# Performance work log

Measured on AMD Instinct MI355X. Metric: run time of the kernel, lower is better.

The kernel has to match this reference:

```python
import jax, jax.numpy as jnp
import numpy as np

B_CAPS, C_CAPS, KSZ, STRIDE, N_ITER = 32, 32, 3, 2, 3


def setup_inputs() -> dict:
    key = jax.random.key(0)
    k1, k2, k3, k4, k5 = jax.random.split(key, 5)
    b, Bc, Cc, Win = 8, B_CAPS, C_CAPS, 13
    pose = 0.5 * jax.random.normal(k1, (b, 16 * Bc, Win, Win), jnp.float32)
    act = 0.05 + 0.9 * jax.random.uniform(k2, (b, Bc, Win, Win), jnp.float32)
    x = jnp.concatenate([pose, act], axis=1)
    W = 0.3 * jax.random.normal(k3, (KSZ, KSZ, Bc, Cc, 4, 4), jnp.float32)
    beta_v = jax.random.normal(k4, (1,), jnp.float32)
    beta_a = jax.random.normal(k5, (1,), jnp.float32)
    lambda_ = jnp.ones((1,), jnp.float32)
    return {"x": x, "W": W, "beta_v": beta_v, "beta_a": beta_a, "lambda_": lambda_}


def _conv_caps(x, W, beta_v, beta_a, lambda_):
    B, C, K, s, n_iter = B_CAPS, C_CAPS, KSZ, STRIDE, N_ITER
    b, Win = x.shape[0], x.shape[2]
    Wout = (Win - K) // s + 1
    # channel layout of pose is (4,4,B) row-major, per the original .view(-1,4,4,B,...)
    pose = x[:, :-B].reshape(b, 4, 4, B, Win, Win)
    act = x[:, -B:]
    ks = jnp.arange(K)
    Iidx = s * jnp.arange(Wout)[None, :] + ks[:, None]  # (K,Wout): i_in = s*x + ki
    Ir = Iidx[:, None, :, None]  # (K,1,Wout,1)
    Ic = Iidx[None, :, None, :]  # (1,K,1,Wout)
    # pose patches: (b,4,4,B,K,K,Wout,Wout); matrix dims are (q=rows, r=cols)
    pp = pose[:, :, :, :, Ir, Ic]
    # votes[n,o,ki,kj,x,y,c,p,r] = sum_q W[ki,kj,o,c,p,q] * pose[n,q,r,o,ki,kj,x,y]
    votes = jnp.einsum('ijocpq,nqroijxy->noijxycpr', W, pp)
    votes = votes.reshape(b, B, K, K, Wout, Wout, C, 16)
    a_patch = act[:, :, Ir, Ic]  # (b,B,K,K,Wout,Wout)
    # original E-step indexes votes at pos = stride*x - i, which is <=0 and wraps
    # (torch negative indexing) to (-ki) % K.  Faithfully reproduce that permutation.
    kperm = (-ks) % K
    votesE = votes[:, :, kperm][:, :, :, kperm]
    # routing weights kept in patch form R[i_in=s*x+ki, j_in=s*y+kj, x, y] -> (ki,kj,x,y);
    # this is exactly the set of R entries the original ever reads or writes.
    Rp = jnp.full((b, B, K, K, Wout, Wout, C), 1.0 / (Wout * Wout * C), x.dtype)
    TWO_PI = np.float32(2.0 * np.pi)
    lam = jnp.reshape(lambda_, ())
    mu = act_out = None
    for it in range(n_iter):
        # ---- M-step ----
        r_hat = Rp * a_patch[..., None]                      # (b,B,K,K,Wo,Wo,C)
        sum_r = r_hat.sum(axis=(1, 2, 3))                    # (b,Wo,Wo,C)
        mu = jnp.einsum('noijxyc,noijxycd->nxycd', r_hat, votes) / sum_r[..., None]
        mu_b = mu[:, None, None, None]                       # (b,1,1,1,Wo,Wo,C,16)
        sigma = jnp.einsum('noijxyc,noijxycd->nxycd', r_hat, (votes - mu_b) ** 2) / sum_r[..., None]
        cost = (beta_v + jnp.log(sigma)) * sum_r[..., None]  # (b,Wo,Wo,C,16)
        act_out = jax.nn.sigmoid(lam * (beta_a - cost.sum(-1)))  # (b,Wo,Wo,C)
        # ---- E-step (skipped on last iter: its R is never read afterwards) ----
        if it < n_iter - 1:
            # original: p = exp(-(V-mu)^2)/sqrt(2*pi*sigma), prod over 16 pose dims
            p = jnp.prod(jnp.exp(-(votesE - mu_b) ** 2) / jnp.sqrt(TWO_PI * sigma[:, None, None, None]), axis=-1)
            p_hat = act_out[:, None, None, None] * p         # (b,B,K,K,Wo,Wo,C)
            T = p_hat.sum(-1)                                # (b,B,K,K,Wo,Wo)
            # normalizer is per (batch, input-type, input-position): scatter-add over
            # all (ki,x),(kj,y) mapping to the same input pixel, summed over C
            D = jnp.zeros((b, B, Win, Win), x.dtype).at[:, :, Ir, Ic].add(T)
            Rp = p_hat / D[:, :, Ir, Ic][..., None]
    mus = mu.transpose(0, 3, 4, 1, 2).reshape(b, C * 16, Wout, Wout)
    acts = act_out.transpose(0, 3, 1, 2)                     # (b,C,Wo,Wo)
    return jnp.concatenate([mus, acts], axis=1)              # (b, C*17, Wo, Wo)


def reference(x, W, beta_v, beta_a, lambda_):
    return _conv_caps(x, W, beta_v, beta_a, lambda_)
```

## Files before the change

kernel.cpp:

```cpp
#include <hip/hip_runtime.h>


typedef float v2f __attribute__((ext_vector_type(2)));
typedef float v4f __attribute__((ext_vector_type(4)));

#define OFF_PHAT 0
#define OFF_D0   2654208
#define OFF_D1   2697472
#define OFF_POST 2740736
#define OFF_ACTT 3432960
#define OFF_WT2  3476224

template <int CTRL>
__device__ __forceinline__ float dppadd(float v) {
  int p = __builtin_amdgcn_update_dpp(0, __float_as_int(v), CTRL, 0xF, 0xF, true);
  return v + __int_as_float(p);
}

__device__ __forceinline__ float wsum64(float v) {
  v = dppadd<0xB1>(v);
  v = dppadd<0x4E>(v);
  v = dppadd<0x141>(v);
  v = dppadd<0x140>(v);
  v = dppadd<0x142>(v);
  v = dppadd<0x143>(v);
  return __int_as_float(__builtin_amdgcn_readlane(__float_as_int(v), 63));
}

__device__ __forceinline__ v2f lo2(v4f a) { return __builtin_shufflevector(a, a, 0, 1); }
__device__ __forceinline__ v2f hi2(v4f a) { return __builtin_shufflevector(a, a, 2, 3); }

__global__ __launch_bounds__(256) void prep_kernel(
    const float* __restrict__ x, const float* __restrict__ Wt,
    float* __restrict__ posT, float* __restrict__ actT,
    float* __restrict__ Wt2, float* __restrict__ Dz) {
  int tid = blockIdx.x * 256 + threadIdx.x;
  if (tid < 692224) {
    int pix = tid % 169; int t = tid / 169;
    int o = t & 31; t >>= 5;
    int d = t & 15; int n = t >> 4;
    float v = x[((size_t)n * 544 + d * 32 + o) * 169 + pix];
    posT[((size_t)(n * 32 + o) * 169 + pix) * 16 + d] = v;
  } else if (tid < 735488) {
    int r = tid - 692224;
    int pix = r % 169; int t = r / 169;
    int o = t & 31; int n = t >> 5;
    float v = x[(size_t)n * 91936 + 86528 + o * 169 + pix];
    actT[((size_t)n * 169 + pix) * 32 + o] = v;
  } else if (tid < 882944) {
    int r = tid - 735488;
    int c = r / 4608; int s = r - c * 4608;
    int ch = s >> 4, d = s & 15;
    Wt2[r] = Wt[(size_t)ch * 512 + c * 16 + d];
  } else {
    Dz[tid - 882944] = 0.f;
  }
}

__global__ __launch_bounds__(256, 4) void em_kernel(
    const float* __restrict__ Wt2, const float* __restrict__ posT,
    const float* __restrict__ actT, float* __restrict__ p_hat,
    const float* __restrict__ Dread, float* __restrict__ Dwrite,
    const float* __restrict__ beta_v, const float* __restrict__ beta_a,
    const float* __restrict__ lambda_, float* __restrict__ out, int mode) {
  __shared__ float sP[288 * 20];
  __shared__ float sE[288];
  __shared__ float sPh[4 * 288];

  const int g = blockIdx.x & 7;
  const int sg = blockIdx.x >> 3;
  const int wave = threadIdx.x >> 6;
  const int lane = threadIdx.x & 63;
  const int c = g * 4 + wave;

  int t = sg;
  const int y = t % 6; t /= 6;
  const int xx = t % 6;
  const int n = t / 6;

  const float bvv = beta_v[0], bav = beta_a[0], lamv = lambda_[0];
  const float* wbase = Wt2 + (size_t)c * 4608;

  float phv[5];
  if (mode != 0) {
    const float* phb = p_hat + ((size_t)sg * 32 + c) * 288;
#pragma unroll
    for (int k = 0; k < 5; ++k) {
      int ch = lane + 64 * k; if (ch > 287) ch = 287;
      phv[k] = phb[ch];
    }
  }

  for (int task = threadIdx.x; task < 1152; task += 256) {
    int ch = task >> 2, q = task & 3;
    int o = ch & 31, ij = ch >> 5;
    int i = ij / 3, j = ij - i * 3;
    int pix = (2 * xx + i) * 13 + (2 * y + j);
    v4f v = *(const v4f*)(posT +
        ((size_t)((n * 32 + o) * 169) + pix) * 16 + q * 4);
    *(v4f*)(sP + ch * 20 + q * 4) = v;
  }
  for (int task = threadIdx.x; task < 288; task += 256) {
    int o = task & 31, ij = task >> 5;
    int i = ij / 3, j = ij - i * 3;
    int idx = ((size_t)n * 169 + (2 * xx + i) * 13 + (2 * y + j)) * 32 + o;
    float a = actT[idx];
    sE[task] = (mode == 0) ? a * (1.0f / 1152.0f) : a / Dread[idx];
  }
  __syncthreads();

  float sum_r = 0.f;
  v2f sv2[8], sq2[8];
#pragma unroll
  for (int d = 0; d < 8; ++d) { sv2[d] = 0.f; sq2[d] = 0.f; }

#pragma unroll
  for (int k = 0; k < 5; ++k) {
    int ch = lane + 64 * k;
    const bool act_l = (ch < 288);
    const int chm = act_l ? ch : 0;

    const v4f* Pp = (const v4f*)(sP + chm * 20);
    v4f P0 = Pp[0], P1 = Pp[1], P2 = Pp[2], P3 = Pp[3];
    const v4f* Wp = (const v4f*)(wbase + chm * 16);
    v4f W0 = Wp[0], W1 = Wp[1], W2 = Wp[2], W3 = Wp[3];

    float rhat = sE[chm];
    if (mode != 0) rhat *= phv[k];
    if (!act_l) rhat = 0.f;
    sum_r += rhat;

    v2f PL0 = lo2(P0), PH0 = hi2(P0), PL1 = lo2(P1), PH1 = hi2(P1);
    v2f PL2 = lo2(P2), PH2 = hi2(P2), PL3 = lo2(P3), PH3 = hi2(P3);
    v2f r2 = rhat;

#pragma unroll
    for (int p = 0; p < 4; ++p) {
      v4f Wr = (p == 0) ? W0 : (p == 1) ? W1 : (p == 2) ? W2 : W3;
      v2f vlo = Wr.x * PL0 + Wr.y * PL1 + Wr.z * PL2 + Wr.w * PL3;
      v2f vhi = Wr.x * PH0 + Wr.y * PH1 + Wr.z * PH2 + Wr.w * PH3;
      v2f tlo = r2 * vlo, thi = r2 * vhi;
      sv2[p * 2 + 0] += tlo;
      sv2[p * 2 + 1] += thi;
      sq2[p * 2 + 0] += tlo * vlo;
      sq2[p * 2 + 1] += thi * vhi;
    }
  }

  sum_r = wsum64(sum_r);
  const float inv_sr = 1.0f / sum_r;
  float mu[16];
  float lsum = 0.f;
#pragma unroll
  for (int d = 0; d < 16; ++d) {
    float s1 = wsum64(sv2[d >> 1][d & 1]);
    float s2 = wsum64(sq2[d >> 1][d & 1]);
    float m = s1 * inv_sr;
    mu[d] = m;
    float sg_ = fmaxf(s2 * inv_sr - m * m, 1e-30f);
    lsum += __logf(sg_);
  }
  const float cost = (16.f * bvv + lsum) * sum_r;
  const float aout = 1.0f / (1.0f + __expf(-lamv * (bav - cost)));

  if (mode == 2) {
    if (lane == 0) {
      float* ob = out + (size_t)(n * 544 + c * 16) * 36 + xx * 6 + y;
#pragma unroll
      for (int d = 0; d < 16; ++d) ob[d * 36] = mu[d];
      out[(size_t)(n * 544 + 512 + c) * 36 + xx * 6 + y] = aout;
    }
    return;
  }

  v2f mu2[8];
#pragma unroll
  for (int d = 0; d < 8; ++d) { mu2[d].x = mu[2 * d]; mu2[d].y = mu[2 * d + 1]; }
  const float G = __logf(aout) - 0.5f * (lsum + 16.f * 1.8378770664093453f);

#pragma unroll
  for (int k = 0; k < 5; ++k) {
    int mch = lane + 64 * k;
    if (mch < 288) {
      const v4f* Pp = (const v4f*)(sP + mch * 20);
      v4f P0 = Pp[0], P1 = Pp[1], P2 = Pp[2], P3 = Pp[3];
      const v4f* Wp = (const v4f*)(wbase + mch * 16);
      v4f W0 = Wp[0], W1 = Wp[1], W2 = Wp[2], W3 = Wp[3];

      v2f PL0 = lo2(P0), PH0 = hi2(P0), PL1 = lo2(P1), PH1 = hi2(P1);
      v2f PL2 = lo2(P2), PH2 = hi2(P2), PL3 = lo2(P3), PH3 = hi2(P3);
      v2f ss2 = 0.f;
#pragma unroll
      for (int p = 0; p < 4; ++p) {
        v4f Wr = (p == 0) ? W0 : (p == 1) ? W1 : (p == 2) ? W2 : W3;
        v2f vlo = Wr.x * PL0 + Wr.y * PL1 + Wr.z * PL2 + Wr.w * PL3;
        v2f vhi = Wr.x * PH0 + Wr.y * PH1 + Wr.z * PH2 + Wr.w * PH3;
        v2f dlo = vlo - mu2[p * 2 + 0];
        v2f dhi = vhi - mu2[p * 2 + 1];
        ss2 += dlo * dlo;
        ss2 += dhi * dhi;
      }
      float ss = ss2.x + ss2.y;
      float ph = __expf(G - ss);
      int o = mch & 31, ijm = mch >> 5;
      int im = ijm / 3, jm = ijm - im * 3;
      int i2 = (im == 0) ? 0 : 3 - im;
      int j2 = (jm == 0) ? 0 : 3 - jm;
      int slot = (i2 * 3 + j2) * 32 + o;
      p_hat[((size_t)sg * 32 + c) * 288 + slot] = ph;
      sPh[wave * 288 + slot] = ph;
    }
  }
  __syncthreads();
  for (int t2 = threadIdx.x; t2 < 288; t2 += 256) {
    float s = sPh[t2] + sPh[288 + t2] + sPh[576 + t2] + sPh[864 + t2];
    int o = t2 & 31, ij = t2 >> 5;
    int i = ij / 3, j = ij - i * 3;
    atomicAdd(Dwrite + ((size_t)n * 169 + (2 * xx + i) * 13 + (2 * y + j)) * 32 + o, s);
  }
}

extern "C" void kernel_launch(void* const* d_in, const int* in_sizes, int n_in,
                              void* d_out, int out_size, void* d_ws,
                              size_t ws_size, hipStream_t stream) {
  const float* x   = (const float*)d_in[0];
  const float* Wt  = (const float*)d_in[1];
  const float* bv  = (const float*)d_in[2];
  const float* ba  = (const float*)d_in[3];
  const float* lam = (const float*)d_in[4];
  float* out = (float*)d_out;
  float* ws = (float*)d_ws;

  float* p_hat = ws + OFF_PHAT;
  float* D0    = ws + OFF_D0;
  float* D1    = ws + OFF_D1;
  float* posT  = ws + OFF_POST;
  float* actT  = ws + OFF_ACTT;
  float* Wt2   = ws + OFF_WT2;

  (void)in_sizes; (void)n_in; (void)out_size; (void)ws_size;

  prep_kernel<<<3787, 256, 0, stream>>>(x, Wt, posT, actT, Wt2, D0);

  em_kernel<<<2304, 256, 0, stream>>>(Wt2, posT, actT, p_hat, D1, D0,
                                      bv, ba, lam, out, 0);
  em_kernel<<<2304, 256, 0, stream>>>(Wt2, posT, actT, p_hat, D0, D1,
                                      bv, ba, lam, out, 1);
  em_kernel<<<2304, 256, 0, stream>>>(Wt2, posT, actT, p_hat, D1, D0,
                                      bv, ba, lam, out, 2);
}
```

Baseline: 155.1 us.

## Pre-gather pose patches per output position and read them directly from global

The prep kernel now writes pose data already gathered into per-output-position patch order (sg, channel, 16), so the EM kernels read their 288×16 pose block contiguously from global memory instead of staging it through shared memory. This removes the LDS fill loop and the 23 KB shared buffer, and halves the occupancy hint in launch bounds. The mode flag becomes a template parameter, and the 16 per-dimension logs are replaced by four logs of products of four variances. In exchange, prep writes a larger duplicated buffer, each wave re-reads the patch through the cache, and products of small variances could underflow.

Result: slower. 172.9 us (+11.5%).

```diff
diff --git a/kernel.cpp b/kernel.cpp
--- a/kernel.cpp
+++ b/kernel.cpp
@@ -7,9 +7,9 @@
 #define OFF_PHAT 0
 #define OFF_D0   2654208
 #define OFF_D1   2697472
-#define OFF_POST 2740736
-#define OFF_ACTT 3432960
-#define OFF_WT2  3476224
+#define OFF_POSP 2740736
+#define OFF_ACTT 4067840
+#define OFF_WT2  4111104
 
 template <int CTRL>
 __device__ __forceinline__ float dppadd(float v) {
@@ -32,38 +32,41 @@
 
 __global__ __launch_bounds__(256) void prep_kernel(
     const float* __restrict__ x, const float* __restrict__ Wt,
-    float* __restrict__ posT, float* __restrict__ actT,
+    float* __restrict__ posP, float* __restrict__ actT,
     float* __restrict__ Wt2, float* __restrict__ Dz) {
   int tid = blockIdx.x * 256 + threadIdx.x;
-  if (tid < 692224) {
-    int pix = tid % 169; int t = tid / 169;
-    int o = t & 31; t >>= 5;
-    int d = t & 15; int n = t >> 4;
-    float v = x[((size_t)n * 544 + d * 32 + o) * 169 + pix];
-    posT[((size_t)(n * 32 + o) * 169 + pix) * 16 + d] = v;
-  } else if (tid < 735488) {
-    int r = tid - 692224;
+  if (tid < 1327104) {
+    int d = tid & 15; int t = tid >> 4;
+    int ch = t % 288; int sg = t / 288;
+    int o = ch & 31, ij = ch >> 5;
+    int i = ij / 3, j = ij - i * 3;
+    int y = sg % 6; int t2 = sg / 6;
+    int xx = t2 % 6; int n = t2 / 6;
+    int pix = (2 * xx + i) * 13 + (2 * y + j);
+    posP[tid] = x[((size_t)n * 544 + d * 32 + o) * 169 + pix];
+  } else if (tid < 1370368) {
+    int r = tid - 1327104;
     int pix = r % 169; int t = r / 169;
     int o = t & 31; int n = t >> 5;
     float v = x[(size_t)n * 91936 + 86528 + o * 169 + pix];
     actT[((size_t)n * 169 + pix) * 32 + o] = v;
-  } else if (tid < 882944) {
-    int r = tid - 735488;
+  } else if (tid < 1517824) {
+    int r = tid - 1370368;
     int c = r / 4608; int s = r - c * 4608;
     int ch = s >> 4, d = s & 15;
     Wt2[r] = Wt[(size_t)ch * 512 + c * 16 + d];
   } else {
-    Dz[tid - 882944] = 0.f;
-  }
-}
-
-__global__ __launch_bounds__(256, 4) void em_kernel(
-    const float* __restrict__ Wt2, const float* __restrict__ posT,
+    Dz[tid - 1517824] = 0.f;
+  }
+}
+
+template <int MODE>
+__global__ __launch_bounds__(256, 2) void em_kernel(
+    const float* __restrict__ Wt2, const float* __restrict__ posP,
     const float* __restrict__ actT, float* __restrict__ p_hat,
     const float* __restrict__ Dread, float* __restrict__ Dwrite,
     const float* __restrict__ beta_v, const float* __restrict__ beta_a,
-    const float* __restrict__ lambda_, float* __restrict__ out, int mode) {
-  __shared__ float sP[288 * 20];
+    const float* __restrict__ lambda_, float* __restrict__ out) {
   __shared__ float sE[288];
   __shared__ float sPh[4 * 288];
 
@@ -80,9 +83,10 @@
 
   const float bvv = beta_v[0], bav = beta_a[0], lamv = lambda_[0];
   const float* wbase = Wt2 + (size_t)c * 4608;
+  const float* pbase = posP + (size_t)sg * 288 * 16;
 
   float phv[5];
-  if (mode != 0) {
+  if (MODE != 0) {
     const float* phb = p_hat + ((size_t)sg * 32 + c) * 288;
 #pragma unroll
     for (int k = 0; k < 5; ++k) {
@@ -91,21 +95,12 @@
     }
   }
 
-  for (int task = threadIdx.x; task < 1152; task += 256) {
-    int ch = task >> 2, q = task & 3;
-    int o = ch & 31, ij = ch >> 5;
-    int i = ij / 3, j = ij - i * 3;
-    int pix = (2 * xx + i) * 13 + (2 * y + j);
-    v4f v = *(const v4f*)(posT +
-        ((size_t)((n * 32 + o) * 169) + pix) * 16 + q * 4);
-    *(v4f*)(sP + ch * 20 + q * 4) = v;
-  }
   for (int task = threadIdx.x; task < 288; task += 256) {
     int o = task & 31, ij = task >> 5;
     int i = ij / 3, j = ij - i * 3;
     int idx = ((size_t)n * 169 + (2 * xx + i) * 13 + (2 * y + j)) * 32 + o;
     float a = actT[idx];
-    sE[task] = (mode == 0) ? a * (1.0f / 1152.0f) : a / Dread[idx];
+    sE[task] = (MODE == 0) ? a * (1.0f / 1152.0f) : a / Dread[idx];
   }
   __syncthreads();
 
@@ -120,13 +115,13 @@
     const bool act_l = (ch < 288);
     const int chm = act_l ? ch : 0;
 
-    const v4f* Pp = (const v4f*)(sP + chm * 20);
+    const v4f* Pp = (const v4f*)(pbase + (size_t)chm * 16);
     v4f P0 = Pp[0], P1 = Pp[1], P2 = Pp[2], P3 = Pp[3];
     const v4f* Wp = (const v4f*)(wbase + chm * 16);
     v4f W0 = Wp[0], W1 = Wp[1], W2 = Wp[2], W3 = Wp[3];
 
     float rhat = sE[chm];
-    if (mode != 0) rhat *= phv[k];
+    if (MODE != 0) rhat *= phv[k];
     if (!act_l) rhat = 0.f;
     sum_r += rhat;
 
@@ -151,6 +146,7 @@
   const float inv_sr = 1.0f / sum_r;
   float mu[16];
   float lsum = 0.f;
+  float prod = 1.f;
 #pragma unroll
   for (int d = 0; d < 16; ++d) {
     float s1 = wsum64(sv2[d >> 1][d & 1]);
@@ -158,12 +154,13 @@
     float m = s1 * inv_sr;
     mu[d] = m;
     float sg_ = fmaxf(s2 * inv_sr - m * m, 1e-30f);
-    lsum += __logf(sg_);
+    prod *= sg_;
+    if ((d & 3) == 3) { lsum += __logf(prod); prod = 1.f; }
   }
   const float cost = (16.f * bvv + lsum) * sum_r;
   const float aout = 1.0f / (1.0f + __expf(-lamv * (bav - cost)));
 
-  if (mode == 2) {
+  if (MODE == 2) {
     if (lane == 0) {
       float* ob = out + (size_t)(n * 544 + c * 16) * 36 + xx * 6 + y;
 #pragma unroll
@@ -182,7 +179,7 @@
   for (int k = 0; k < 5; ++k) {
     int mch = lane + 64 * k;
     if (mch < 288) {
-      const v4f* Pp = (const v4f*)(sP + mch * 20);
+      const v4f* Pp = (const v4f*)(pbase + (size_t)mch * 16);
       v4f P0 = Pp[0], P1 = Pp[1], P2 = Pp[2], P3 = Pp[3];
       const v4f* Wp = (const v4f*)(wbase + mch * 16);
       v4f W0 = Wp[0], W1 = Wp[1], W2 = Wp[2], W3 = Wp[3];
@@ -234,18 +231,18 @@
   float* p_hat = ws + OFF_PHAT;
   float* D0    = ws + OFF_D0;
   float* D1    = ws + OFF_D1;
-  float* posT  = ws + OFF_POST;
+  float* posP  = ws + OFF_POSP;
   float* actT  = ws + OFF_ACTT;
   float* Wt2   = ws + OFF_WT2;
 
   (void)in_sizes; (void)n_in; (void)out_size; (void)ws_size;
 
-  prep_kernel<<<3787, 256, 0, stream>>>(x, Wt, posT, actT, Wt2, D0);
-
-  em_kernel<<<2304, 256, 0, stream>>>(Wt2, posT, actT, p_hat, D1, D0,
-                                      bv, ba, lam, out, 0);
-  em_kernel<<<2304, 256, 0, stream>>>(Wt2, posT, actT, p_hat, D0, D1,
-                                      bv, ba, lam, out, 1);
-  em_kernel<<<2304, 256, 0, stream>>>(Wt2, posT, actT, p_hat, D1, D0,
-                                      bv, ba, lam, out, 2);
-}
+  prep_kernel<<<6267, 256, 0, stream>>>(x, Wt, posP, actT, Wt2, D0);
+
+  em_kernel<0><<<2304, 256, 0, stream>>>(Wt2, posP, actT, p_hat, D1, D0,
+                                         bv, ba, lam, out);
+  em_kernel<1><<<2304, 256, 0, stream>>>(Wt2, posP, actT, p_hat, D0, D1,
+                                         bv, ba, lam, out);
+  em_kernel<2><<<2304, 256, 0, stream>>>(Wt2, posP, actT, p_hat, D1, D0,
+                                         bv, ba, lam, out);
+}
```

## Lane-interleave weight layout, templatize mode, batch log calls in EM kernel

Applied to the files above, without the earlier changes.

Reorders the per-class weight tensor so each wave lane reads consecutive 16-byte chunks (coalesced v4f loads indexed by lane), padding channels past 288 with zeros. It also makes the mode a template parameter so dead branches compile out, relaxes launch bounds from 4 to 2 blocks per CU (more registers, possibly lower occupancy), and multiplies groups of four variances before taking a single log. The layout targets strided uncoalesced weight loads from global memory. The product of four variances could lose accuracy if the values are extreme.

Result: faster. 143.2 us (-7.6%).

```diff
diff --git a/kernel.cpp b/kernel.cpp
--- a/kernel.cpp
+++ b/kernel.cpp
@@ -9,7 +9,7 @@
 #define OFF_D1   2697472
 #define OFF_POST 2740736
 #define OFF_ACTT 3432960
-#define OFF_WT2  3476224
+#define OFF_WT3  3476224
 
 template <int CTRL>
 __device__ __forceinline__ float dppadd(float v) {
@@ -33,7 +33,7 @@
 __global__ __launch_bounds__(256) void prep_kernel(
     const float* __restrict__ x, const float* __restrict__ Wt,
     float* __restrict__ posT, float* __restrict__ actT,
-    float* __restrict__ Wt2, float* __restrict__ Dz) {
+    float* __restrict__ Wt3, float* __restrict__ Dz) {
   int tid = blockIdx.x * 256 + threadIdx.x;
   if (tid < 692224) {
     int pix = tid % 169; int t = tid / 169;
@@ -47,22 +47,27 @@
     int o = t & 31; int n = t >> 5;
     float v = x[(size_t)n * 91936 + 86528 + o * 169 + pix];
     actT[((size_t)n * 169 + pix) * 32 + o] = v;
-  } else if (tid < 882944) {
+  } else if (tid < 899328) {
     int r = tid - 735488;
-    int c = r / 4608; int s = r - c * 4608;
-    int ch = s >> 4, d = s & 15;
-    Wt2[r] = Wt[(size_t)ch * 512 + c * 16 + d];
+    int j = r & 3;
+    int lane = (r >> 2) & 63;
+    int q = (r >> 8) & 3;
+    int rem = r >> 10;
+    int k = rem % 5; int c = rem / 5;
+    int ch = 64 * k + lane;
+    Wt3[r] = (ch < 288) ? Wt[(size_t)ch * 512 + c * 16 + 4 * q + j] : 0.f;
   } else {
-    Dz[tid - 882944] = 0.f;
-  }
-}
-
-__global__ __launch_bounds__(256, 4) void em_kernel(
-    const float* __restrict__ Wt2, const float* __restrict__ posT,
+    Dz[tid - 899328] = 0.f;
+  }
+}
+
+template <int MODE>
+__global__ __launch_bounds__(256, 2) void em_kernel(
+    const float* __restrict__ Wt3, const float* __restrict__ posT,
     const float* __restrict__ actT, float* __restrict__ p_hat,
     const float* __restrict__ Dread, float* __restrict__ Dwrite,
     const float* __restrict__ beta_v, const float* __restrict__ beta_a,
-    const float* __restrict__ lambda_, float* __restrict__ out, int mode) {
+    const float* __restrict__ lambda_, float* __restrict__ out) {
   __shared__ float sP[288 * 20];
   __shared__ float sE[288];
   __shared__ float sPh[4 * 288];
@@ -79,10 +84,10 @@
   const int n = t / 6;
 
   const float bvv = beta_v[0], bav = beta_a[0], lamv = lambda_[0];
-  const float* wbase = Wt2 + (size_t)c * 4608;
+  const float* wbase = Wt3 + (size_t)c * 5120;
 
   float phv[5];
-  if (mode != 0) {
+  if (MODE != 0) {
     const float* phb = p_hat + ((size_t)sg * 32 + c) * 288;
 #pragma unroll
     for (int k = 0; k < 5; ++k) {
@@ -105,7 +110,7 @@
     int i = ij / 3, j = ij - i * 3;
     int idx = ((size_t)n * 169 + (2 * xx + i) * 13 + (2 * y + j)) * 32 + o;
     float a = actT[idx];
-    sE[task] = (mode == 0) ? a * (1.0f / 1152.0f) : a / Dread[idx];
+    sE[task] = (MODE == 0) ? a * (1.0f / 1152.0f) : a / Dread[idx];
   }
   __syncthreads();
 
@@ -122,11 +127,11 @@
 
     const v4f* Pp = (const v4f*)(sP + chm * 20);
     v4f P0 = Pp[0], P1 = Pp[1], P2 = Pp[2], P3 = Pp[3];
-    const v4f* Wp = (const v4f*)(wbase + chm * 16);
-    v4f W0 = Wp[0], W1 = Wp[1], W2 = Wp[2], W3 = Wp[3];
+    const v4f* Wq = (const v4f*)(wbase + k * 1024);
+    v4f W0 = Wq[lane], W1 = Wq[64 + lane], W2 = Wq[128 + lane], W3 = Wq[192 + lane];
 
     float rhat = sE[chm];
-    if (mode != 0) rhat *= phv[k];
+    if (MODE != 0) rhat *= phv[k];
     if (!act_l) rhat = 0.f;
     sum_r += rhat;
 
@@ -151,6 +156,7 @@
   const float inv_sr = 1.0f / sum_r;
   float mu[16];
   float lsum = 0.f;
+  float prod = 1.f;
 #pragma unroll
   for (int d = 0; d < 16; ++d) {
     float s1 = wsum64(sv2[d >> 1][d & 1]);
@@ -158,12 +164,13 @@
     float m = s1 * inv_sr;
     mu[d] = m;
     float sg_ = fmaxf(s2 * inv_sr - m * m, 1e-30f);
-    lsum += __logf(sg_);
+    prod *= sg_;
+    if ((d & 3) == 3) { lsum += __logf(prod); prod = 1.f; }
   }
   const float cost = (16.f * bvv + lsum) * sum_r;
   const float aout = 1.0f / (1.0f + __expf(-lamv * (bav - cost)));
 
-  if (mode == 2) {
+  if (MODE == 2) {
     if (lane == 0) {
       float* ob = out + (size_t)(n * 544 + c * 16) * 36 + xx * 6 + y;
 #pragma unroll
@@ -184,8 +191,8 @@
     if (mch < 288) {
       const v4f* Pp = (const v4f*)(sP + mch * 20);
       v4f P0 = Pp[0], P1 = Pp[1], P2 = Pp[2], P3 = Pp[3];
-      const v4f* Wp = (const v4f*)(wbase + mch * 16);
-      v4f W0 = Wp[0], W1 = Wp[1], W2 = Wp[2], W3 = Wp[3];
+      const v4f* Wq = (const v4f*)(wbase + k * 1024);
+      v4f W0 = Wq[lane], W1 = Wq[64 + lane], W2 = Wq[128 + lane], W3 = Wq[192 + lane];
 
       v2f PL0 = lo2(P0), PH0 = hi2(P0), PL1 = lo2(P1), PH1 = hi2(P1);
       v2f PL2 = lo2(P2), PH2 = hi2(P2), PL3 = lo2(P3), PH3 = hi2(P3);
@@ -236,16 +243,16 @@
   float* D1    = ws + OFF_D1;
   float* posT  = ws + OFF_POST;
   float* actT  = ws + OFF_ACTT;
-  float* Wt2   = ws + OFF_WT2;
+  float* Wt3   = ws + OFF_WT3;
 
   (void)in_sizes; (void)n_in; (void)out_size; (void)ws_size;
 
-  prep_kernel<<<3787, 256, 0, stream>>>(x, Wt, posT, actT, Wt2, D0);
-
-  em_kernel<<<2304, 256, 0, stream>>>(Wt2, posT, actT, p_hat, D1, D0,
-                                      bv, ba, lam, out, 0);
-  em_kernel<<<2304, 256, 0, stream>>>(Wt2, posT, actT, p_hat, D0, D1,
-                                      bv, ba, lam, out, 1);
-  em_kernel<<<2304, 256, 0, stream>>>(Wt2, posT, actT, p_hat, D1, D0,
-                                      bv, ba, lam, out, 2);
-}
+  prep_kernel<<<3851, 256, 0, stream>>>(x, Wt, posT, actT, Wt3, D0);
+
+  em_kernel<0><<<2304, 256, 0, stream>>>(Wt3, posT, actT, p_hat, D1, D0,
+                                         bv, ba, lam, out);
+  em_kernel<1><<<2304, 256, 0, stream>>>(Wt3, posT, actT, p_hat, D0, D1,
+                                         bv, ba, lam, out);
+  em_kernel<2><<<2304, 256, 0, stream>>>(Wt3, posT, actT, p_hat, D1, D0,
+                                         bv, ba, lam, out);
+}
```
